# Performance work log

Hardware: AMD Instinct MI355X
Metric: run time of the kernel (lower is better)

The kernel has to match this reference:

```python
import jax, jax.numpy as jnp
import numpy as np

B, H, KVH, D = 64, 32, 8, 128     # batch, q heads, kv heads, head dim
BS, MB = 16, 128                  # paged-cache block size, max blocks per seq
NB = B * MB                       # total cache blocks (8192)
L = MB * BS                       # max kv length per sequence (2048)
SCALE = 0.08838834764831845       # 1/sqrt(head_dim)


def setup_inputs() -> dict:
    key = jax.random.key(0)
    ks = jax.random.split(key, 6)
    q = jax.random.normal(ks[0], (B, H * D), jnp.float32)
    k = jax.random.normal(ks[1], (B, KVH * D), jnp.float32)
    v = jax.random.normal(ks[2], (B, KVH * D), jnp.float32)
    k_cache = jax.random.normal(ks[3], (NB, BS, KVH, D), jnp.float32)
    v_cache = jax.random.normal(ks[4], (NB, BS, KVH, D), jnp.float32)
    # each sequence owns MB disjoint contiguous blocks
    block_tables = jnp.arange(B * MB, dtype=jnp.int32).reshape(B, MB)
    context_lens = jax.random.randint(ks[5], (B,), 0, L - 1, dtype=jnp.int32)
    return dict(q=q, k=k, v=v, k_cache=k_cache, v_cache=v_cache,
                block_tables=block_tables, context_lens=context_lens)


def reference(q, k, v, k_cache, v_cache, block_tables, context_lens):
    G = H // KVH  # GQA group size
    qh = q.reshape(B, KVH, G, D)
    kh = k.reshape(B, KVH, D)
    vh = v.reshape(B, KVH, D)
    # store new token's KV at its paged slot (position = context_len)
    slots = block_tables[jnp.arange(B), context_lens // BS] * BS + context_lens % BS
    kc = k_cache.reshape(NB * BS, KVH, D).at[slots].set(kh)
    vc = v_cache.reshape(NB * BS, KVH, D).at[slots].set(vh)
    # gather paged KV per sequence via block tables -> [B, L, KVH, D]
    keys = kc.reshape(NB, BS, KVH, D)[block_tables].reshape(B, L, KVH, D)
    vals = vc.reshape(NB, BS, KVH, D)[block_tables].reshape(B, L, KVH, D)
    # GQA attention: each kv head serves G query heads
    scores = jnp.einsum('bkgd,blkd->bkgl', qh, keys) * SCALE
    valid = jnp.arange(L)[None, :] <= context_lens[:, None]  # [B, L], inclusive of new token
    scores = jnp.where(valid[:, None, None, :], scores, jnp.float32(-jnp.inf))
    w = jax.nn.softmax(scores, axis=-1)
    out = jnp.einsum('bkgl,blkd->bkgd', w, vals)
    return out.reshape(B, H * D)
```

## Files before the change

kernel.cpp:

```cpp
#include <hip/hip_runtime.h>

#define BATCH 64
#define NHEADS 32
#define KVH 8
#define HDIM 128
#define GQA 4
#define BLKSZ 16
#define MAXBLK 128
#define MAXLEN 2048
#define SCALE 0.08838834764831845f

#define CHUNK 64
#define NPART (MAXLEN / CHUNK)
#define GSTRIDE 132
#define SLOT_BYTES 4096u
#define WS_FLOATS ((size_t)BATCH * NPART * KVH * GQA * GSTRIDE)

typedef unsigned int uint;

struct KVBuf { float4 k0, k1, v0, v1; };

__global__ __launch_bounds__(256, 4) void pa_partial(
    const float* __restrict__ q,
    const float* __restrict__ knew,
    const float* __restrict__ vnew,
    const float* __restrict__ k_cache,
    const float* __restrict__ v_cache,
    const int*   __restrict__ block_tables,
    const int*   __restrict__ context_lens,
    float* __restrict__ ws)
{
    const int bid  = blockIdx.x;
    const int part = bid & (NPART - 1);
    const int b    = bid >> 5;

    const int cl = context_lens[b];
    const int n  = cl + 1;
    const int p0 = part * CHUNK;
    if (p0 >= n) return;
    const int pend = min(p0 + CHUNK, n);

    const int tid  = threadIdx.x;
    const int kvh  = tid >> 5;
    const int lane = tid & 31;
    const uint laneByte = ((uint)kvh << 9) + ((uint)lane << 4);

    float4 qf[GQA];
    #pragma unroll
    for (int g = 0; g < GQA; ++g) {
        float4 t = *reinterpret_cast<const float4*>(
            &q[(size_t)b * (NHEADS * HDIM) + (size_t)(kvh * GQA + g) * HDIM + lane * 4]);
        t.x *= SCALE; t.y *= SCALE; t.z *= SCALE; t.w *= SCALE;
        qf[g] = t;
    }

    float  s[GQA];
    float4 acc[GQA];
    #pragma unroll
    for (int g = 0; g < GQA; ++g) {
        s[g] = 0.f;
        acc[g] = make_float4(0.f, 0.f, 0.f, 0.f);
    }

    const char* kc8 = reinterpret_cast<const char*>(k_cache);
    const char* vc8 = reinterpret_cast<const char*>(v_cache);

    if (p0 + CHUNK <= cl) {
        int blkv[4];
        #pragma unroll
        for (int c = 0; c < 4; ++c)
            blkv[c] = block_tables[b * MAXBLK + (p0 >> 4) + c];

        KVBuf bufA, bufB;

#define ISSUE(P, i)                                                              \
        {                                                                        \
            const uint u0 = ((uint)blkv[(2*(i)) >> 4] * BLKSZ + ((2*(i)) & 15)) * SLOT_BYTES + laneByte; \
            const uint u1 = ((uint)blkv[(2*(i)+1) >> 4] * BLKSZ + ((2*(i)+1) & 15)) * SLOT_BYTES + laneByte; \
            buf##P.k0 = *reinterpret_cast<const float4*>(kc8 + u0);              \
            buf##P.k1 = *reinterpret_cast<const float4*>(kc8 + u1);              \
            buf##P.v0 = *reinterpret_cast<const float4*>(vc8 + u0);              \
            buf##P.v1 = *reinterpret_cast<const float4*>(vc8 + u1);              \
        }

#define CONSUME(P)                                                               \
        {                                                                        \
            float sc0[GQA], sc1[GQA];                                            \
            _Pragma("unroll")                                                    \
            for (int g = 0; g < GQA; ++g) {                                      \
                sc0[g] = buf##P.k0.x * qf[g].x + buf##P.k0.y * qf[g].y           \
                       + buf##P.k0.z * qf[g].z + buf##P.k0.w * qf[g].w;          \
                sc1[g] = buf##P.k1.x * qf[g].x + buf##P.k1.y * qf[g].y           \
                       + buf##P.k1.z * qf[g].z + buf##P.k1.w * qf[g].w;          \
            }                                                                    \
            _Pragma("unroll")                                                    \
            for (int off = 16; off > 0; off >>= 1) {                             \
                _Pragma("unroll")                                                \
                for (int g = 0; g < GQA; ++g) {                                  \
                    sc0[g] += __shfl_xor(sc0[g], off, 32);                       \
                    sc1[g] += __shfl_xor(sc1[g], off, 32);                       \
                }                                                                \
            }                                                                    \
            _Pragma("unroll")                                                    \
            for (int g = 0; g < GQA; ++g) {                                      \
                const float e0 = __expf(sc0[g]);                                 \
                const float e1 = __expf(sc1[g]);                                 \
                s[g] += e0 + e1;                                                 \
                acc[g].x += e0 * buf##P.v0.x + e1 * buf##P.v1.x;                 \
                acc[g].y += e0 * buf##P.v0.y + e1 * buf##P.v1.y;                 \
                acc[g].z += e0 * buf##P.v0.z + e1 * buf##P.v1.z;                 \
                acc[g].w += e0 * buf##P.v0.w + e1 * buf##P.v1.w;                 \
            }                                                                    \
        }

        ISSUE(A, 0);
        #pragma unroll
        for (int i = 0; i < 31; ++i) {
            if (i & 1) { ISSUE(A, i + 1); CONSUME(B); }
            else       { ISSUE(B, i + 1); CONSUME(A); }
        }
        CONSUME(B);
#undef ISSUE
#undef CONSUME
    } else {
        const int* bt = &block_tables[b * MAXBLK];
        const float* knrow = &knew[((size_t)b * KVH + kvh) * HDIM + lane * 4];
        const float* vnrow = &vnew[((size_t)b * KVH + kvh) * HDIM + lane * 4];

        for (int t0 = p0; t0 < pend; t0 += 4) {
            bool valid[4];
            const float* kp[4];
            const float* vp[4];
            #pragma unroll
            for (int j = 0; j < 4; ++j) {
                const int l = t0 + j;
                valid[j] = (l < pend);
                if (!valid[j] || l == cl) {
                    kp[j] = knrow; vp[j] = vnrow;
                } else {
                    const int blk = bt[l >> 4];
                    const uint u  = ((uint)blk * BLKSZ + (l & 15)) * SLOT_BYTES + laneByte;
                    kp[j] = reinterpret_cast<const float*>(kc8 + u);
                    vp[j] = reinterpret_cast<const float*>(vc8 + u);
                }
            }

            float4 kf[4], vf[4];
            #pragma unroll
            for (int j = 0; j < 4; ++j) kf[j] = *reinterpret_cast<const float4*>(kp[j]);
            #pragma unroll
            for (int j = 0; j < 4; ++j) vf[j] = *reinterpret_cast<const float4*>(vp[j]);

            float sc[4][GQA];
            #pragma unroll
            for (int j = 0; j < 4; ++j)
                #pragma unroll
                for (int g = 0; g < GQA; ++g)
                    sc[j][g] = kf[j].x * qf[g].x + kf[j].y * qf[g].y
                             + kf[j].z * qf[g].z + kf[j].w * qf[g].w;

            #pragma unroll
            for (int off = 16; off > 0; off >>= 1)
                #pragma unroll
                for (int j = 0; j < 4; ++j)
                    #pragma unroll
                    for (int g = 0; g < GQA; ++g)
                        sc[j][g] += __shfl_xor(sc[j][g], off, 32);

            #pragma unroll
            for (int g = 0; g < GQA; ++g) {
                float p[4];
                #pragma unroll
                for (int j = 0; j < 4; ++j)
                    p[j] = valid[j] ? __expf(sc[j][g]) : 0.f;
                s[g] += (p[0] + p[1]) + (p[2] + p[3]);
                acc[g].x += p[0] * vf[0].x + p[1] * vf[1].x + p[2] * vf[2].x + p[3] * vf[3].x;
                acc[g].y += p[0] * vf[0].y + p[1] * vf[1].y + p[2] * vf[2].y + p[3] * vf[3].y;
                acc[g].z += p[0] * vf[0].z + p[1] * vf[1].z + p[2] * vf[2].z + p[3] * vf[3].z;
                acc[g].w += p[0] * vf[0].w + p[1] * vf[1].w + p[2] * vf[2].w + p[3] * vf[3].w;
            }
        }
    }

    float* rec = ws + ((size_t)(bid * KVH + kvh) * GQA) * GSTRIDE;
    #pragma unroll
    for (int g = 0; g < GQA; ++g)
        *reinterpret_cast<float4*>(rec + (size_t)g * GSTRIDE + lane * 4) = acc[g];
    if (lane == 0) {
        #pragma unroll
        for (int g = 0; g < GQA; ++g) rec[(size_t)g * GSTRIDE + 128] = s[g];
    }
}

__global__ __launch_bounds__(128) void pa_reduce(
    const float* __restrict__ ws,
    const int*   __restrict__ context_lens,
    float* __restrict__ out)
{
    const int bid = blockIdx.x;
    const int b   = bid >> 5;
    const int kvh = (bid >> 2) & 7;
    const int g   = bid & 3;
    const int d   = threadIdx.x;

    const int n    = context_lens[b] + 1;
    const int pcnt = (n + CHUNK - 1) / CHUNK;

    const float* base = ws + ((size_t)(b * NPART * KVH + kvh) * GQA + g) * GSTRIDE;
    const size_t pstride = (size_t)KVH * GQA * GSTRIDE;

    float O0 = 0.f, O1 = 0.f, O2 = 0.f, O3 = 0.f;
    float S0 = 0.f, S1 = 0.f, S2 = 0.f, S3 = 0.f;
    int p = 0;
    for (; p + 4 <= pcnt; p += 4) {
        const float* r0 = base + (p + 0) * pstride;
        const float* r1 = base + (p + 1) * pstride;
        const float* r2 = base + (p + 2) * pstride;
        const float* r3 = base + (p + 3) * pstride;
        O0 += r0[d]; O1 += r1[d]; O2 += r2[d]; O3 += r3[d];
        S0 += r0[128]; S1 += r1[128]; S2 += r2[128]; S3 += r3[128];
    }
    for (; p < pcnt; ++p) {
        const float* r = base + p * pstride;
        O0 += r[d]; S0 += r[128];
    }
    const float O = (O0 + O1) + (O2 + O3);
    const float S = (S0 + S1) + (S2 + S3);

    out[(size_t)b * (NHEADS * HDIM) + (size_t)(kvh * GQA + g) * HDIM + d] = O / S;
}

__global__ __launch_bounds__(256) void paged_attn_decode(
    const float* __restrict__ q,
    const float* __restrict__ knew,
    const float* __restrict__ vnew,
    const float* __restrict__ k_cache,
    const float* __restrict__ v_cache,
    const int*   __restrict__ block_tables,
    const int*   __restrict__ context_lens,
    float* __restrict__ out)
{
    const int bh   = blockIdx.x;
    const int b    = bh / KVH;
    const int kvh  = bh % KVH;
    const int tid  = threadIdx.x;
    const int hw   = tid >> 5;
    const int lane = tid & 31;

    const int cl = context_lens[b];
    const int n  = cl + 1;

    float4 qf[GQA];
    #pragma unroll
    for (int g = 0; g < GQA; ++g) {
        float4 t = *reinterpret_cast<const float4*>(
            &q[(size_t)b * (NHEADS * HDIM) + (size_t)(kvh * GQA + g) * HDIM + lane * 4]);
        t.x *= SCALE; t.y *= SCALE; t.z *= SCALE; t.w *= SCALE;
        qf[g] = t;
    }

    float  s[GQA];
    float4 acc[GQA];
    #pragma unroll
    for (int g = 0; g < GQA; ++g) { s[g] = 0.f; acc[g] = make_float4(0.f,0.f,0.f,0.f); }

    const int* bt = &block_tables[b * MAXBLK];

    for (int l = hw; l < n; l += 8) {
        const float4* krow;
        const float4* vrow;
        if (l == cl) {
            krow = reinterpret_cast<const float4*>(&knew[(size_t)(b * KVH + kvh) * HDIM]);
            vrow = reinterpret_cast<const float4*>(&vnew[(size_t)(b * KVH + kvh) * HDIM]);
        } else {
            const int    blk = bt[l >> 4];
            const size_t off = (((size_t)blk * BLKSZ + (l & 15)) * KVH + kvh) * HDIM;
            krow = reinterpret_cast<const float4*>(&k_cache[off]);
            vrow = reinterpret_cast<const float4*>(&v_cache[off]);
        }
        const float4 kf = krow[lane];
        const float4 vf = vrow[lane];

        float sc[GQA];
        #pragma unroll
        for (int g = 0; g < GQA; ++g)
            sc[g] = kf.x * qf[g].x + kf.y * qf[g].y + kf.z * qf[g].z + kf.w * qf[g].w;

        #pragma unroll
        for (int off = 16; off > 0; off >>= 1)
            #pragma unroll
            for (int g = 0; g < GQA; ++g)
                sc[g] += __shfl_xor(sc[g], off, 32);

        #pragma unroll
        for (int g = 0; g < GQA; ++g) {
            const float p = __expf(sc[g]);
            s[g] += p;
            acc[g].x += p * vf.x; acc[g].y += p * vf.y;
            acc[g].z += p * vf.z; acc[g].w += p * vf.w;
        }
    }

    __shared__ float lds_s[8][GQA];
    __shared__ float lds_acc[8][GQA][HDIM];

    #pragma unroll
    for (int g = 0; g < GQA; ++g)
        *reinterpret_cast<float4*>(&lds_acc[hw][g][lane * 4]) = acc[g];
    if (lane == 0) {
        #pragma unroll
        for (int g = 0; g < GQA; ++g) lds_s[hw][g] = s[g];
    }
    __syncthreads();

    for (int i = tid; i < GQA * HDIM; i += 256) {
        const int g = i >> 7;
        const int d = i & 127;
        float S = 0.f, O = 0.f;
        #pragma unroll
        for (int h = 0; h < 8; ++h) { S += lds_s[h][g]; O += lds_acc[h][g][d]; }
        out[(size_t)b * (NHEADS * HDIM) + (size_t)(kvh * GQA + g) * HDIM + d] = O / S;
    }
}

extern "C" void kernel_launch(void* const* d_in, const int* in_sizes, int n_in,
                              void* d_out, int out_size, void* d_ws, size_t ws_size,
                              hipStream_t stream) {
    const float* q      = (const float*)d_in[0];
    const float* k      = (const float*)d_in[1];
    const float* v      = (const float*)d_in[2];
    const float* kc     = (const float*)d_in[3];
    const float* vc     = (const float*)d_in[4];
    const int*   bt     = (const int*)d_in[5];
    const int*   clens  = (const int*)d_in[6];
    float*       out    = (float*)d_out;

    if (ws_size >= WS_FLOATS * sizeof(float)) {
        float* ws = (float*)d_ws;
        pa_partial<<<dim3(BATCH * NPART), dim3(256), 0, stream>>>(
            q, k, v, kc, vc, bt, clens, ws);
        pa_reduce<<<dim3(BATCH * KVH * GQA), dim3(128), 0, stream>>>(ws, clens, out);
    } else {
        paged_attn_decode<<<dim3(BATCH * KVH), dim3(256), 0, stream>>>(
            q, k, v, kc, vc, bt, clens, out);
    }
}
```

Baseline: 145.4 us.

## Use persistent blocks with an atomic work queue for partial attention chunks

Replaces the one-block-per-(batch,chunk) grid with 1024 persistent blocks that pull work items from a global atomic counter, reset by a tiny init kernel. Blocks whose chunk lies beyond the context length now skip ahead cheaply instead of launching empty blocks, and load balances dynamically. It adds an extra kernel launch, two barriers plus an atomic per item, and serialises per-block work.

After: 174.5 us. +20.0%, slower.

```diff
diff --git a/kernel.cpp b/kernel.cpp
--- a/kernel.cpp
+++ b/kernel.cpp
@@ -12,13 +12,17 @@
 
 #define CHUNK 64
 #define NPART (MAXLEN / CHUNK)
+#define NITEMS (BATCH * NPART)
 #define GSTRIDE 132
 #define SLOT_BYTES 4096u
-#define WS_FLOATS ((size_t)BATCH * NPART * KVH * GQA * GSTRIDE)
+#define WS_FLOATS ((size_t)NITEMS * KVH * GQA * GSTRIDE)
+#define NBLOCKS 1024
 
 typedef unsigned int uint;
 
 struct KVBuf { float4 k0, k1, v0, v1; };
+
+__global__ void pa_init(uint* __restrict__ qcnt) { *qcnt = 0u; }
 
 __global__ __launch_bounds__(256, 4) void pa_partial(
     const float* __restrict__ q,
@@ -28,167 +32,177 @@
     const float* __restrict__ v_cache,
     const int*   __restrict__ block_tables,
     const int*   __restrict__ context_lens,
-    float* __restrict__ ws)
+    float* __restrict__ ws,
+    uint*  __restrict__ qcnt)
 {
-    const int bid  = blockIdx.x;
-    const int part = bid & (NPART - 1);
-    const int b    = bid >> 5;
-
-    const int cl = context_lens[b];
-    const int n  = cl + 1;
-    const int p0 = part * CHUNK;
-    if (p0 >= n) return;
-    const int pend = min(p0 + CHUNK, n);
-
     const int tid  = threadIdx.x;
     const int kvh  = tid >> 5;
     const int lane = tid & 31;
     const uint laneByte = ((uint)kvh << 9) + ((uint)lane << 4);
 
-    float4 qf[GQA];
-    #pragma unroll
-    for (int g = 0; g < GQA; ++g) {
-        float4 t = *reinterpret_cast<const float4*>(
-            &q[(size_t)b * (NHEADS * HDIM) + (size_t)(kvh * GQA + g) * HDIM + lane * 4]);
-        t.x *= SCALE; t.y *= SCALE; t.z *= SCALE; t.w *= SCALE;
-        qf[g] = t;
-    }
-
-    float  s[GQA];
-    float4 acc[GQA];
-    #pragma unroll
-    for (int g = 0; g < GQA; ++g) {
-        s[g] = 0.f;
-        acc[g] = make_float4(0.f, 0.f, 0.f, 0.f);
-    }
-
     const char* kc8 = reinterpret_cast<const char*>(k_cache);
     const char* vc8 = reinterpret_cast<const char*>(v_cache);
 
-    if (p0 + CHUNK <= cl) {
-        int blkv[4];
-        #pragma unroll
-        for (int c = 0; c < 4; ++c)
-            blkv[c] = block_tables[b * MAXBLK + (p0 >> 4) + c];
-
-        KVBuf bufA, bufB;
+    __shared__ int s_item;
+
+    for (;;) {
+        __syncthreads();
+        if (tid == 0) s_item = (int)atomicAdd(qcnt, 1u);
+        __syncthreads();
+        const int item = s_item;
+        if (item >= NITEMS) break;
+
+        const int part = item & (NPART - 1);
+        const int b    = item >> 5;
+
+        const int cl = context_lens[b];
+        const int n  = cl + 1;
+        const int p0 = part * CHUNK;
+        if (p0 >= n) continue;
+        const int pend = min(p0 + CHUNK, n);
+
+        float4 qf[GQA];
+        #pragma unroll
+        for (int g = 0; g < GQA; ++g) {
+            float4 t = *reinterpret_cast<const float4*>(
+                &q[(size_t)b * (NHEADS * HDIM) + (size_t)(kvh * GQA + g) * HDIM + lane * 4]);
+            t.x *= SCALE; t.y *= SCALE; t.z *= SCALE; t.w *= SCALE;
+            qf[g] = t;
+        }
+
+        float  s[GQA];
+        float4 acc[GQA];
+        #pragma unroll
+        for (int g = 0; g < GQA; ++g) {
+            s[g] = 0.f;
+            acc[g] = make_float4(0.f, 0.f, 0.f, 0.f);
+        }
+
+        if (p0 + CHUNK <= cl) {
+            int blkv[4];
+            #pragma unroll
+            for (int c = 0; c < 4; ++c)
+                blkv[c] = block_tables[b * MAXBLK + (p0 >> 4) + c];
+
+            KVBuf bufA, bufB;
 
 #define ISSUE(P, i)                                                              \
-        {                                                                        \
-            const uint u0 = ((uint)blkv[(2*(i)) >> 4] * BLKSZ + ((2*(i)) & 15)) * SLOT_BYTES + laneByte; \
-            const uint u1 = ((uint)blkv[(2*(i)+1) >> 4] * BLKSZ + ((2*(i)+1) & 15)) * SLOT_BYTES + laneByte; \
-            buf##P.k0 = *reinterpret_cast<const float4*>(kc8 + u0);              \
-            buf##P.k1 = *reinterpret_cast<const float4*>(kc8 + u1);              \
-            buf##P.v0 = *reinterpret_cast<const float4*>(vc8 + u0);              \
-            buf##P.v1 = *reinterpret_cast<const float4*>(vc8 + u1);              \
-        }
+            {                                                                    \
+                const uint u0 = ((uint)blkv[(2*(i)) >> 4] * BLKSZ + ((2*(i)) & 15)) * SLOT_BYTES + laneByte; \
+                const uint u1 = ((uint)blkv[(2*(i)+1) >> 4] * BLKSZ + ((2*(i)+1) & 15)) * SLOT_BYTES + laneByte; \
+                buf##P.k0 = *reinterpret_cast<const float4*>(kc8 + u0);          \
+                buf##P.k1 = *reinterpret_cast<const float4*>(kc8 + u1);          \
+                buf##P.v0 = *reinterpret_cast<const float4*>(vc8 + u0);          \
+                buf##P.v1 = *reinterpret_cast<const float4*>(vc8 + u1);          \
+            }
 
 #define CONSUME(P)                                                               \
-        {                                                                        \
-            float sc0[GQA], sc1[GQA];                                            \
-            _Pragma("unroll")                                                    \
-            for (int g = 0; g < GQA; ++g) {                                      \
-                sc0[g] = buf##P.k0.x * qf[g].x + buf##P.k0.y * qf[g].y           \
-                       + buf##P.k0.z * qf[g].z + buf##P.k0.w * qf[g].w;          \
-                sc1[g] = buf##P.k1.x * qf[g].x + buf##P.k1.y * qf[g].y           \
-                       + buf##P.k1.z * qf[g].z + buf##P.k1.w * qf[g].w;          \
-            }                                                                    \
-            _Pragma("unroll")                                                    \
-            for (int off = 16; off > 0; off >>= 1) {                             \
+            {                                                                    \
+                float sc0[GQA], sc1[GQA];                                        \
                 _Pragma("unroll")                                                \
                 for (int g = 0; g < GQA; ++g) {                                  \
-                    sc0[g] += __shfl_xor(sc0[g], off, 32);                       \
-                    sc1[g] += __shfl_xor(sc1[g], off, 32);                       \
+                    sc0[g] = buf##P.k0.x * qf[g].x + buf##P.k0.y * qf[g].y       \
+                           + buf##P.k0.z * qf[g].z + buf##P.k0.w * qf[g].w;      \
+                    sc1[g] = buf##P.k1.x * qf[g].x + buf##P.k1.y * qf[g].y       \
+                           + buf##P.k1.z * qf[g].z + buf##P.k1.w * qf[g].w;      \
                 }                                                                \
-            }                                                                    \
-            _Pragma("unroll")                                                    \
-            for (int g = 0; g < GQA; ++g) {                                      \
-                const float e0 = __expf(sc0[g]);                                 \
-                const float e1 = __expf(sc1[g]);                                 \
-                s[g] += e0 + e1;                                                 \
-                acc[g].x += e0 * buf##P.v0.x + e1 * buf##P.v1.x;                 \
-                acc[g].y += e0 * buf##P.v0.y + e1 * buf##P.v1.y;                 \
-                acc[g].z += e0 * buf##P.v0.z + e1 * buf##P.v1.z;                 \
-                acc[g].w += e0 * buf##P.v0.w + e1 * buf##P.v1.w;                 \
-            }                                                                    \
-        }
-
-        ISSUE(A, 0);
-        #pragma unroll
-        for (int i = 0; i < 31; ++i) {
-            if (i & 1) { ISSUE(A, i + 1); CONSUME(B); }
-            else       { ISSUE(B, i + 1); CONSUME(A); }
-        }
-        CONSUME(B);
+                _Pragma("unroll")                                                \
+                for (int off = 16; off > 0; off >>= 1) {                         \
+                    _Pragma("unroll")                                            \
+                    for (int g = 0; g < GQA; ++g) {                              \
+                        sc0[g] += __shfl_xor(sc0[g], off, 32);                   \
+                        sc1[g] += __shfl_xor(sc1[g], off, 32);                   \
+                    }                                                            \
+                }                                                                \
+                _Pragma("unroll")                                                \
+                for (int g = 0; g < GQA; ++g) {                                  \
+                    const float e0 = __expf(sc0[g]);                             \
+                    const float e1 = __expf(sc1[g]);                             \
+                    s[g] += e0 + e1;                                             \
+                    acc[g].x += e0 * buf##P.v0.x + e1 * buf##P.v1.x;             \
+                    acc[g].y += e0 * buf##P.v0.y + e1 * buf##P.v1.y;             \
+                    acc[g].z += e0 * buf##P.v0.z + e1 * buf##P.v1.z;             \
+                    acc[g].w += e0 * buf##P.v0.w + e1 * buf##P.v1.w;             \
+                }                                                                \
+            }
+
+            ISSUE(A, 0);
+            #pragma unroll
+            for (int i = 0; i < 31; ++i) {
+                if (i & 1) { ISSUE(A, i + 1); CONSUME(B); }
+                else       { ISSUE(B, i + 1); CONSUME(A); }
+            }
+            CONSUME(B);
 #undef ISSUE
 #undef CONSUME
-    } else {
-        const int* bt = &block_tables[b * MAXBLK];
-        const float* knrow = &knew[((size_t)b * KVH + kvh) * HDIM + lane * 4];
-        const float* vnrow = &vnew[((size_t)b * KVH + kvh) * HDIM + lane * 4];
-
-        for (int t0 = p0; t0 < pend; t0 += 4) {
-            bool valid[4];
-            const float* kp[4];
-            const float* vp[4];
-            #pragma unroll
-            for (int j = 0; j < 4; ++j) {
-                const int l = t0 + j;
-                valid[j] = (l < pend);
-                if (!valid[j] || l == cl) {
-                    kp[j] = knrow; vp[j] = vnrow;
-                } else {
-                    const int blk = bt[l >> 4];
-                    const uint u  = ((uint)blk * BLKSZ + (l & 15)) * SLOT_BYTES + laneByte;
-                    kp[j] = reinterpret_cast<const float*>(kc8 + u);
-                    vp[j] = reinterpret_cast<const float*>(vc8 + u);
+        } else {
+            const int* bt = &block_tables[b * MAXBLK];
+            const float* knrow = &knew[((size_t)b * KVH + kvh) * HDIM + lane * 4];
+            const float* vnrow = &vnew[((size_t)b * KVH + kvh) * HDIM + lane * 4];
+
+            for (int t0 = p0; t0 < pend; t0 += 4) {
+                bool valid[4];
+                const float* kp[4];
+                const float* vp[4];
+                #pragma unroll
+                for (int j = 0; j < 4; ++j) {
+                    const int l = t0 + j;
+                    valid[j] = (l < pend);
+                    if (!valid[j] || l == cl) {
+                        kp[j] = knrow; vp[j] = vnrow;
+                    } else {
+                        const int blk = bt[l >> 4];
+                        const uint u  = ((uint)blk * BLKSZ + (l & 15)) * SLOT_BYTES + laneByte;
+                        kp[j] = reinterpret_cast<const float*>(kc8 + u);
+                        vp[j] = reinterpret_cast<const float*>(vc8 + u);
+                    }
                 }
-            }
-
-            float4 kf[4], vf[4];
-            #pragma unroll
-            for (int j = 0; j < 4; ++j) kf[j] = *reinterpret_cast<const float4*>(kp[j]);
-            #pragma unroll
-            for (int j = 0; j < 4; ++j) vf[j] = *reinterpret_cast<const float4*>(vp[j]);
-
-            float sc[4][GQA];
-            #pragma unroll
-            for (int j = 0; j < 4; ++j)
-                #pragma unroll
-                for (int g = 0; g < GQA; ++g)
-                    sc[j][g] = kf[j].x * qf[g].x + kf[j].y * qf[g].y
-                             + kf[j].z * qf[g].z + kf[j].w * qf[g].w;
-
-            #pragma unroll
-            for (int off = 16; off > 0; off >>= 1)
+
+                float4 kf[4], vf[4];
+                #pragma unroll
+                for (int j = 0; j < 4; ++j) kf[j] = *reinterpret_cast<const float4*>(kp[j]);
+                #pragma unroll
+                for (int j = 0; j < 4; ++j) vf[j] = *reinterpret_cast<const float4*>(vp[j]);
+
+                float sc[4][GQA];
                 #pragma unroll
                 for (int j = 0; j < 4; ++j)
                     #pragma unroll
                     for (int g = 0; g < GQA; ++g)
-                        sc[j][g] += __shfl_xor(sc[j][g], off, 32);
-
+                        sc[j][g] = kf[j].x * qf[g].x + kf[j].y * qf[g].y
+                                 + kf[j].z * qf[g].z + kf[j].w * qf[g].w;
+
+                #pragma unroll
+                for (int off = 16; off > 0; off >>= 1)
+                    #pragma unroll
+                    for (int j = 0; j < 4; ++j)
+                        #pragma unroll
+                        for (int g = 0; g < GQA; ++g)
+                            sc[j][g] += __shfl_xor(sc[j][g], off, 32);
+
+                #pragma unroll
+                for (int g = 0; g < GQA; ++g) {
+                    float p[4];
+                    #pragma unroll
+                    for (int j = 0; j < 4; ++j)
+                        p[j] = valid[j] ? __expf(sc[j][g]) : 0.f;
+                    s[g] += (p[0] + p[1]) + (p[2] + p[3]);
+                    acc[g].x += p[0] * vf[0].x + p[1] * vf[1].x + p[2] * vf[2].x + p[3] * vf[3].x;
+                    acc[g].y += p[0] * vf[0].y + p[1] * vf[1].y + p[2] * vf[2].y + p[3] * vf[3].y;
+                    acc[g].z += p[0] * vf[0].z + p[1] * vf[1].z + p[2] * vf[2].z + p[3] * vf[3].z;
+                    acc[g].w += p[0] * vf[0].w + p[1] * vf[1].w + p[2] * vf[2].w + p[3] * vf[3].w;
+                }
+            }
+        }
+
+        float* rec = ws + ((size_t)(item * KVH + kvh) * GQA) * GSTRIDE;
+        #pragma unroll
+        for (int g = 0; g < GQA; ++g)
+            *reinterpret_cast<float4*>(rec + (size_t)g * GSTRIDE + lane * 4) = acc[g];
+        if (lane == 0) {
             #pragma unroll
-            for (int g = 0; g < GQA; ++g) {
-                float p[4];
-                #pragma unroll
-                for (int j = 0; j < 4; ++j)
-                    p[j] = valid[j] ? __expf(sc[j][g]) : 0.f;
-                s[g] += (p[0] + p[1]) + (p[2] + p[3]);
-                acc[g].x += p[0] * vf[0].x + p[1] * vf[1].x + p[2] * vf[2].x + p[3] * vf[3].x;
-                acc[g].y += p[0] * vf[0].y + p[1] * vf[1].y + p[2] * vf[2].y + p[3] * vf[3].y;
-                acc[g].z += p[0] * vf[0].z + p[1] * vf[1].z + p[2] * vf[2].z + p[3] * vf[3].z;
-                acc[g].w += p[0] * vf[0].w + p[1] * vf[1].w + p[2] * vf[2].w + p[3] * vf[3].w;
-            }
-        }
-    }
-
-    float* rec = ws + ((size_t)(bid * KVH + kvh) * GQA) * GSTRIDE;
-    #pragma unroll
-    for (int g = 0; g < GQA; ++g)
-        *reinterpret_cast<float4*>(rec + (size_t)g * GSTRIDE + lane * 4) = acc[g];
-    if (lane == 0) {
-        #pragma unroll
-        for (int g = 0; g < GQA; ++g) rec[(size_t)g * GSTRIDE + 128] = s[g];
+            for (int g = 0; g < GQA; ++g) rec[(size_t)g * GSTRIDE + 128] = s[g];
+        }
     }
 }
 
@@ -206,7 +220,7 @@
     const int n    = context_lens[b] + 1;
     const int pcnt = (n + CHUNK - 1) / CHUNK;
 
-    const float* base = ws + ((size_t)(b * NPART * KVH + kvh) * GQA + g) * GSTRIDE;
+    const float* base = ws + ((size_t)((b * NPART) * KVH + kvh) * GQA + g) * GSTRIDE;
     const size_t pstride = (size_t)KVH * GQA * GSTRIDE;
 
     float O0 = 0.f, O1 = 0.f, O2 = 0.f, O3 = 0.f;
@@ -335,10 +349,12 @@
     const int*   clens  = (const int*)d_in[6];
     float*       out    = (float*)d_out;
 
-    if (ws_size >= WS_FLOATS * sizeof(float)) {
-        float* ws = (float*)d_ws;
-        pa_partial<<<dim3(BATCH * NPART), dim3(256), 0, stream>>>(
-            q, k, v, kc, vc, bt, clens, ws);
+    if (ws_size >= (WS_FLOATS + 16) * sizeof(float)) {
+        float* ws   = (float*)d_ws;
+        uint*  qcnt = (uint*)(ws + WS_FLOATS);
+        pa_init<<<dim3(1), dim3(1), 0, stream>>>(qcnt);
+        pa_partial<<<dim3(NBLOCKS), dim3(256), 0, stream>>>(
+            q, k, v, kc, vc, bt, clens, ws, qcnt);
         pa_reduce<<<dim3(BATCH * KVH * GQA), dim3(128), 0, stream>>>(ws, clens, out);
     } else {
         paged_attn_decode<<<dim3(BATCH * KVH), dim3(256), 0, stream>>>(
```
